# Kernel optimization log

Measured on AMD Instinct MI355X. Metric: run time of the kernel, lower is better.

The kernel has to match this reference:

```python
import jax, jax.numpy as jnp
import numpy as np

LN_EPS = 1e-5
OPM_EPS = 1e-3


def setup_inputs() -> dict:
    key = jax.random.key(0)
    ks = jax.random.split(key, 8)
    S, N, c_m, c_h, c_z = 128, 256, 256, 32, 128
    m = jax.random.normal(ks[0], (S, N, c_m), dtype=jnp.float32)
    mask = jnp.ones((S, N), dtype=jnp.float32)
    ln_w = jnp.ones((c_m,), dtype=jnp.float32)
    ln_b = jnp.zeros((c_m,), dtype=jnp.float32)
    sc1 = 1.0 / np.sqrt(c_m)
    w1 = jax.random.uniform(ks[1], (c_m, c_h), jnp.float32, -sc1, sc1)
    b1 = jax.random.uniform(ks[2], (c_h,), jnp.float32, -sc1, sc1)
    w2 = jax.random.uniform(ks[3], (c_m, c_h), jnp.float32, -sc1, sc1)
    b2 = jax.random.uniform(ks[4], (c_h,), jnp.float32, -sc1, sc1)
    sco = 1.0 / np.sqrt(c_h * c_h)
    wo = jax.random.uniform(ks[5], (c_h * c_h, c_z), jnp.float32, -sco, sco)
    bo = jax.random.uniform(ks[6], (c_z,), jnp.float32, -sco, sco)
    return {"m": m, "mask": mask, "ln_w": ln_w, "ln_b": ln_b,
            "w1": w1, "b1": b1, "w2": w2, "b2": b2, "wo": wo, "bo": bo}


def reference(m, mask, ln_w, ln_b, w1, b1, w2, b2, wo, bo):
    # LayerNorm over c_m
    mu = jnp.mean(m, axis=-1, keepdims=True)
    var = jnp.var(m, axis=-1, keepdims=True)
    ln = (m - mu) * jax.lax.rsqrt(var + LN_EPS) * ln_w + ln_b
    mk = mask[..., None]                       # [S, N, 1]
    a = (ln @ w1 + b1) * mk                    # [S, N, c_h]
    b = (ln @ w2 + b2) * mk                    # [S, N, c_h]
    # outer-product mean over the MSA dim s: [N, N, c_h, c_h]
    S, N, ch = a.shape
    outer = jnp.einsum('sic,sjd->ijcd', a, b).reshape(N, N, ch * ch)
    outer = outer @ wo + bo                    # [N, N, c_z]
    norm = jnp.einsum('si,sj->ij', mask, mask)[..., None] + OPM_EPS
    return outer / norm
```

## Files before the change

### kernel.cpp

```cpp
#include <hip/hip_runtime.h>
#include <hip/hip_bf16.h>

typedef __attribute__((ext_vector_type(8))) short short8;
typedef __attribute__((ext_vector_type(4))) short short4v;
typedef __attribute__((ext_vector_type(4))) float float4v;

#define S_DIM 128
#define N_DIM 256
#define CM    256
#define CH    32
#define CZ    128

#define AS1 __attribute__((address_space(1)))
#define AS3 __attribute__((address_space(3)))

static __device__ __forceinline__ short f2bf(float v) {
    return __builtin_bit_cast(short, __float2bfloat16(v));
}


__global__ __launch_bounds__(256) void prep_aux_kernel(
    const float* __restrict__ m, const float* __restrict__ mask,
    const float* __restrict__ lnw, const float* __restrict__ lnb,
    const float* __restrict__ w1, const float* __restrict__ b1,
    const float* __restrict__ w2, const float* __restrict__ b2,
    const float* __restrict__ wo, const float* __restrict__ bo,
    __hip_bfloat16* __restrict__ a_f, __hip_bfloat16* __restrict__ b_f,
    __hip_bfloat16* __restrict__ wo_f, float* __restrict__ ninv)
{
    __shared__ __align__(16) char lds_raw[77824];
    __hip_bfloat16* ln_lds = (__hip_bfloat16*)lds_raw;
    __hip_bfloat16* w_lds  = (__hip_bfloat16*)(lds_raw + 33792);
    __hip_bfloat16* st_lds = (__hip_bfloat16*)(lds_raw + 67584);

    const int bid = blockIdx.x, t = threadIdx.x;

    if (bid >= 576) {
        int i0 = (bid - 576) * 4, j = t;
        float a0 = 0.f, a1 = 0.f, a2 = 0.f, a3 = 0.f;
        for (int s = 0; s < S_DIM; ++s) {
            float mj = mask[s * N_DIM + j];
            a0 += mask[s * N_DIM + i0 + 0] * mj;
            a1 += mask[s * N_DIM + i0 + 1] * mj;
            a2 += mask[s * N_DIM + i0 + 2] * mj;
            a3 += mask[s * N_DIM + i0 + 3] * mj;
        }
        ninv[(i0 + 0) * N_DIM + j] = 1.0f / (a0 + 1e-3f);
        ninv[(i0 + 1) * N_DIM + j] = 1.0f / (a1 + 1e-3f);
        ninv[(i0 + 2) * N_DIM + j] = 1.0f / (a2 + 1e-3f);
        ninv[(i0 + 3) * N_DIM + j] = 1.0f / (a3 + 1e-3f);
        return;
    }
    if (bid >= 512) {
        int fidx = (bid - 512) * 256 + t;
        int l  = fidx & 63;
        int d  = (fidx >> 6) & 31;
        int zt = fidx >> 11;
        int z  = zt * 16 + (l & 15);
        int cb = (l >> 4) * 8;
        short8 frag;
        #pragma unroll
        for (int j = 0; j < 8; ++j)
            frag[j] = f2bf(wo[(size_t)((cb + j) * 32 + d) * CZ + z]);
        *(short8*)&wo_f[(size_t)fidx * 8] = frag;
        return;
    }

    const int lane = t & 63, wv = t >> 6;
    const int q = lane >> 4, c16 = lane & 15;
    const int n0 = (bid & 127) * 2, s0 = (bid >> 7) * 32, sk = bid >> 7;

    #pragma unroll 4
    for (int i = 0; i < 64; ++i) {
        int e = i * 256 + t;
        int k = e >> 6, c = e & 63;
        float v = (c < CH) ? w1[k * CH + c] : w2[k * CH + (c - CH)];
        w_lds[c * 264 + k] = __float2bfloat16(v);
    }

    float4 lw = ((const float4*)lnw)[lane];
    float4 lb = ((const float4*)lnb)[lane];

    #pragma unroll 2
    for (int it = 0; it < 16; ++it) {
        int rl = wv * 16 + it;
        int r  = (s0 + (rl >> 1)) * N_DIM + n0 + (rl & 1);
        float4 mv = ((const float4*)(m + (size_t)r * CM))[lane];
        float s1 = mv.x + mv.y + mv.z + mv.w;
        float s2 = mv.x*mv.x + mv.y*mv.y + mv.z*mv.z + mv.w*mv.w;
        #pragma unroll
        for (int o = 32; o > 0; o >>= 1) {
            s1 += __shfl_xor(s1, o, 64);
            s2 += __shfl_xor(s2, o, 64);
        }
        float mu  = s1 * (1.0f / 256.0f);
        float var = s2 * (1.0f / 256.0f) - mu * mu;
        float rs  = rsqrtf(var + 1e-5f);
        int base = rl * 264 + lane * 4;
        ln_lds[base + 0] = __float2bfloat16((mv.x - mu) * rs * lw.x + lb.x);
        ln_lds[base + 1] = __float2bfloat16((mv.y - mu) * rs * lw.y + lb.y);
        ln_lds[base + 2] = __float2bfloat16((mv.z - mu) * rs * lw.z + lb.z);
        ln_lds[base + 3] = __float2bfloat16((mv.w - mu) * rs * lw.w + lb.w);
    }
    __syncthreads();

    float4v acc[4];
    #pragma unroll
    for (int ct = 0; ct < 4; ++ct) acc[ct] = (float4v){0.f, 0.f, 0.f, 0.f};
    #pragma unroll
    for (int ks = 0; ks < 8; ++ks) {
        int k0 = ks * 32 + q * 8;
        short8 af = *(const short8*)&ln_lds[(wv * 16 + c16) * 264 + k0];
        #pragma unroll
        for (int ct = 0; ct < 4; ++ct) {
            short8 wb = *(const short8*)&w_lds[(ct * 16 + c16) * 264 + k0];
            acc[ct] = __builtin_amdgcn_mfma_f32_16x16x32_bf16(af, wb, acc[ct], 0, 0, 0);
        }
    }

    #pragma unroll
    for (int ct = 0; ct < 4; ++ct) {
        int cc = ct * 16 + c16;
        float bias = (cc < CH) ? b1[cc] : b2[cc - CH];
        #pragma unroll
        for (int rr = 0; rr < 4; ++rr) {
            int rl = wv * 16 + q * 4 + rr;
            int r  = (s0 + (rl >> 1)) * N_DIM + n0 + (rl & 1);
            float val = (acc[ct][rr] + bias) * mask[r];
            st_lds[((rl & 1) * 64 + cc) * 40 + (rl >> 1)] = __float2bfloat16(val);
        }
    }
    __syncthreads();

    #pragma unroll
    for (int i = 0; i < 2; ++i) {
        int slot = i * 256 + t;
        int f8 = slot >> 6, l = slot & 63;
        int fl = f8 & 3, nl = fl >> 1, cch = fl & 1;
        int lq = l >> 4, lc16 = l & 15;
        int col = nl * 64 + (f8 >= 4 ? 32 : 0) + cch * 16 + lc16;
        short8 v = *(const short8*)&st_lds[col * 40 + lq * 8];
        __hip_bfloat16* base = (f8 >= 4) ? b_f : a_f;
        *(short8*)&base[(size_t)((n0 * 2 + fl) * 4 + sk) * 512 + l * 8] = v;
    }
}

__global__ __launch_bounds__(512, 4) void main_kernel(
    const __hip_bfloat16* __restrict__ a_f, const __hip_bfloat16* __restrict__ b_f,
    const __hip_bfloat16* __restrict__ wo_f, const float* __restrict__ bo,
    const float* __restrict__ ninv, float* __restrict__ out)
{
    __shared__ __align__(16) short lds[33280];

    const int t = threadIdx.x, l = t & 63, wv = t >> 6;
    const int q = l >> 4, c16 = l & 15;
    const int bi = blockIdx.x, bj0 = blockIdx.y * 2;
    const size_t Ix = (size_t)bi * 8;

    #pragma unroll
    for (int tau = 0; tau < 2; ++tau) {
        const size_t Jx = (size_t)(bj0 + tau) * 8;
        #pragma unroll
        for (int i = 0; i < 4; ++i) {
            int f = i * 8 + wv;
            __builtin_amdgcn_global_load_lds(
                (AS1 const void*)&b_f[((Jx + (f >> 2)) * 4 + (f & 3)) * 512 + l * 8],
                (AS3 void*)&lds[tau * 16640 + f * 512], 16, 0, 0);
        }
    }

    const int tauW = wv & 1, Ig = (wv >> 1) & 1, Jg = wv >> 2;
    const int RB = tauW * 16640;

    float4v acc[4][4];
    #pragma unroll
    for (int ii = 0; ii < 4; ++ii)
        #pragma unroll
        for (int jj = 0; jj < 4; ++jj)
            acc[ii][jj] = (float4v){0.f, 0.f, 0.f, 0.f};

    __syncthreads();

    #pragma unroll 1
    for (int sk = 0; sk < 4; ++sk) {
        short8 afr[4], bfr[4];
        #pragma unroll
        for (int ii = 0; ii < 4; ++ii)
            afr[ii] = *(const short8*)&a_f[((Ix + Ig * 4 + ii) * 4 + sk) * 512 + l * 8];
        #pragma unroll
        for (int jj = 0; jj < 4; ++jj)
            bfr[jj] = *(const short8*)&lds[RB + ((Jg * 4 + jj) * 4 + sk) * 512 + l * 8];
        #pragma unroll
        for (int jj = 0; jj < 4; ++jj)
            #pragma unroll
            for (int ii = 0; ii < 4; ++ii)
                acc[ii][jj] = __builtin_amdgcn_mfma_f32_16x16x32_bf16(afr[ii], bfr[jj], acc[ii][jj], 0, 0, 0);
    }
    __syncthreads();

    #pragma unroll
    for (int ii = 0; ii < 4; ++ii) {
        const int c0 = (ii & 1) * 16 + q * 4;
        #pragma unroll
        for (int jj = 0; jj < 4; ++jj) {
            const int d = (jj & 1) * 16 + c16;
            const int p = (Ig * 2 + (ii >> 1)) * 4 + Jg * 2 + (jj >> 1);
            short4v pk;
            #pragma unroll
            for (int rr = 0; rr < 4; ++rr) pk[rr] = f2bf(acc[ii][jj][rr]);
            *(short4v*)&lds[RB + d * 520 + (c0 >> 3) * 128 + p * 8 + (c0 & 7)] = pk;
        }
    }
    __syncthreads();

    const int zt = wv & 3, kh = wv >> 2;
    float4v oa00 = (float4v){0.f, 0.f, 0.f, 0.f};
    float4v oa01 = oa00, oa10 = oa00, oa11 = oa00;
    #pragma unroll 2
    for (int d16 = 0; d16 < 16; ++d16) {
        const int d = kh * 16 + d16;
        short8 p0 = *(const short8*)&lds[d * 520 + l * 8];
        short8 p1 = *(const short8*)&lds[16640 + d * 520 + l * 8];
        short8 w0 = *(const short8*)&wo_f[(size_t)(zt * 64 + d) * 512 + l * 8];
        short8 w1 = *(const short8*)&wo_f[(size_t)(zt * 64 + 32 + d) * 512 + l * 8];
        oa00 = __builtin_amdgcn_mfma_f32_16x16x32_bf16(p0, w0, oa00, 0, 0, 0);
        oa01 = __builtin_amdgcn_mfma_f32_16x16x32_bf16(p0, w1, oa01, 0, 0, 0);
        oa10 = __builtin_amdgcn_mfma_f32_16x16x32_bf16(p1, w0, oa10, 0, 0, 0);
        oa11 = __builtin_amdgcn_mfma_f32_16x16x32_bf16(p1, w1, oa11, 0, 0, 0);
    }
    __syncthreads();

    float* red = (float*)lds;
    const int slot = (zt * 64 + l) * 4;
    if (kh) {
        *(float4v*)&red[slot]        = oa00;
        *(float4v*)&red[1024 + slot] = oa01;
    } else {
        *(float4v*)&red[2048 + slot] = oa10;
        *(float4v*)&red[3072 + slot] = oa11;
    }
    __syncthreads();

    float4v f0, f1;
    if (kh == 0) {
        f0 = oa00 + *(const float4v*)&red[slot];
        f1 = oa01 + *(const float4v*)&red[1024 + slot];
    } else {
        f0 = oa10 + *(const float4v*)&red[2048 + slot];
        f1 = oa11 + *(const float4v*)&red[3072 + slot];
    }

    const int gi = bi * 4 + q;
    const int bj = bj0 + kh;
    const int z0 = zt * 32 + c16;
    const float bz0 = bo[z0], bz1 = bo[z0 + 16];
    #pragma unroll
    for (int rr = 0; rr < 4; ++rr) {
        const int gj = bj * 4 + rr;
        const float nv = ninv[gi * N_DIM + gj];
        float* o = &out[((size_t)gi * N_DIM + gj) * CZ + z0];
        o[0]  = (f0[rr] + bz0) * nv;
        o[16] = (f1[rr] + bz1) * nv;
    }
}

extern "C" void kernel_launch(void* const* d_in, const int* in_sizes, int n_in,
                              void* d_out, int out_size, void* d_ws, size_t ws_size,
                              hipStream_t stream) {
    const float* m    = (const float*)d_in[0];
    const float* mask = (const float*)d_in[1];
    const float* lnw  = (const float*)d_in[2];
    const float* lnb  = (const float*)d_in[3];
    const float* w1   = (const float*)d_in[4];
    const float* b1   = (const float*)d_in[5];
    const float* w2   = (const float*)d_in[6];
    const float* b2   = (const float*)d_in[7];
    const float* wo   = (const float*)d_in[8];
    const float* bo   = (const float*)d_in[9];
    float* out = (float*)d_out;

    char* ws = (char*)d_ws;
    __hip_bfloat16* a_f  = (__hip_bfloat16*)ws;
    __hip_bfloat16* b_f  = (__hip_bfloat16*)(ws + (2u << 20));
    __hip_bfloat16* wo_f = (__hip_bfloat16*)(ws + (4u << 20));
    float*          ninv = (float*)(ws + (4u << 20) + (256u << 10));

    prep_aux_kernel<<<640, 256, 0, stream>>>(m, mask, lnw, lnb, w1, b1, w2, b2,
                                             wo, bo, a_f, b_f, wo_f, ninv);
    main_kernel<<<dim3(64, 32), 512, 0, stream>>>(a_f, b_f, wo_f, bo, ninv, out);
}
```

Before: 144.5 us.

## Enlarge main kernel tile to 8x8 residue pairs for operand reuse

```diff
diff --git a/kernel.cpp b/kernel.cpp
--- a/kernel.cpp
+++ b/kernel.cpp
@@ -145,122 +145,140 @@
     }
 }
 
-__global__ __launch_bounds__(512, 4) void main_kernel(
+__global__ __launch_bounds__(512, 2) void main_kernel(
     const __hip_bfloat16* __restrict__ a_f, const __hip_bfloat16* __restrict__ b_f,
     const __hip_bfloat16* __restrict__ wo_f, const float* __restrict__ bo,
     const float* __restrict__ ninv, float* __restrict__ out)
 {
-    __shared__ __align__(16) short lds[33280];
+    __shared__ __align__(16) short lds[66560];
 
     const int t = threadIdx.x, l = t & 63, wv = t >> 6;
     const int q = l >> 4, c16 = l & 15;
-    const int bi = blockIdx.x, bj0 = blockIdx.y * 2;
-    const size_t Ix = (size_t)bi * 8;
-
-    #pragma unroll
-    for (int tau = 0; tau < 2; ++tau) {
-        const size_t Jx = (size_t)(bj0 + tau) * 8;
-        #pragma unroll
-        for (int i = 0; i < 4; ++i) {
-            int f = i * 8 + wv;
-            __builtin_amdgcn_global_load_lds(
-                (AS1 const void*)&b_f[((Jx + (f >> 2)) * 4 + (f & 3)) * 512 + l * 8],
-                (AS3 void*)&lds[tau * 16640 + f * 512], 16, 0, 0);
-        }
-    }
-
-    const int tauW = wv & 1, Ig = (wv >> 1) & 1, Jg = wv >> 2;
-    const int RB = tauW * 16640;
-
-    float4v acc[4][4];
+    const int bi = blockIdx.x, bj = blockIdx.y;
+    const size_t Ix = (size_t)bi * 16;
+    const size_t Jx = (size_t)bj * 16;
+
+    #pragma unroll
+    for (int i = 0; i < 8; ++i) {
+        int f = i * 8 + wv;
+        __builtin_amdgcn_global_load_lds(
+            (AS1 const void*)&b_f[((Jx + (f >> 2)) * 4 + (f & 3)) * 512 + l * 8],
+            (AS3 void*)&lds[f * 512], 16, 0, 0);
+    }
+
+    const int wr = wv & 1, wc = wv >> 1;
+
+    short8 af[4][4];
     #pragma unroll
     for (int ii = 0; ii < 4; ++ii)
         #pragma unroll
-        for (int jj = 0; jj < 4; ++jj)
-            acc[ii][jj] = (float4v){0.f, 0.f, 0.f, 0.f};
-
-    __syncthreads();
-
-    #pragma unroll 1
-    for (int sk = 0; sk < 4; ++sk) {
-        short8 afr[4], bfr[4];
+        for (int sk = 0; sk < 4; ++sk)
+            af[ii][sk] = *(const short8*)&a_f[((Ix + wr * 4 + ii) * 4 + sk) * 512 + l * 8];
+
+    __syncthreads();
+
+    #pragma unroll
+    for (int h = 0; h < 2; ++h) {
+        float4v acc[4][4];
         #pragma unroll
         for (int ii = 0; ii < 4; ++ii)
-            afr[ii] = *(const short8*)&a_f[((Ix + Ig * 4 + ii) * 4 + sk) * 512 + l * 8];
-        #pragma unroll
-        for (int jj = 0; jj < 4; ++jj)
-            bfr[jj] = *(const short8*)&lds[RB + ((Jg * 4 + jj) * 4 + sk) * 512 + l * 8];
-        #pragma unroll
-        for (int jj = 0; jj < 4; ++jj)
+            #pragma unroll
+            for (int jj = 0; jj < 4; ++jj)
+                acc[ii][jj] = (float4v){0.f, 0.f, 0.f, 0.f};
+
+        #pragma unroll 1
+        for (int sk = 0; sk < 4; ++sk) {
+            short8 bfr[4];
+            #pragma unroll
+            for (int jj = 0; jj < 4; ++jj)
+                bfr[jj] = *(const short8*)&lds[((wc * 4 + jj) * 4 + sk) * 512 + l * 8];
+            #pragma unroll
+            for (int jj = 0; jj < 4; ++jj)
+                #pragma unroll
+                for (int ii = 0; ii < 4; ++ii)
+                    acc[ii][jj] = __builtin_amdgcn_mfma_f32_16x16x32_bf16(af[ii][sk], bfr[jj], acc[ii][jj], 0, 0, 0);
+        }
+
+        if (h == 0) {
             #pragma unroll
             for (int ii = 0; ii < 4; ++ii)
-                acc[ii][jj] = __builtin_amdgcn_mfma_f32_16x16x32_bf16(afr[ii], bfr[jj], acc[ii][jj], 0, 0, 0);
-    }
-    __syncthreads();
-
-    #pragma unroll
-    for (int ii = 0; ii < 4; ++ii) {
-        const int c0 = (ii & 1) * 16 + q * 4;
-        #pragma unroll
-        for (int jj = 0; jj < 4; ++jj) {
-            const int d = (jj & 1) * 16 + c16;
-            const int p = (Ig * 2 + (ii >> 1)) * 4 + Jg * 2 + (jj >> 1);
-            short4v pk;
-            #pragma unroll
-            for (int rr = 0; rr < 4; ++rr) pk[rr] = f2bf(acc[ii][jj][rr]);
-            *(short4v*)&lds[RB + d * 520 + (c0 >> 3) * 128 + p * 8 + (c0 & 7)] = pk;
+                #pragma unroll
+                for (int sk = 0; sk < 4; ++sk)
+                    af[ii][sk] = *(const short8*)&a_f[((Ix + 8 + wr * 4 + ii) * 4 + sk) * 512 + l * 8];
+        } else {
+            __syncthreads();
+        }
+
+        const int ib = h * 4;
+        #pragma unroll
+        for (int ii = 0; ii < 4; ++ii) {
+            const int i_loc = ib + ((wr * 4 + ii) >> 1);
+            const int c0 = (ii & 1) * 16 + q * 4;
+            #pragma unroll
+            for (int jj = 0; jj < 4; ++jj) {
+                const int j_loc = (wc * 4 + jj) >> 1;
+                const int d = (jj & 1) * 16 + c16;
+                const int pair = i_loc * 8 + j_loc;
+                const int pf = pair >> 4, p = pair & 15;
+                short4v pk;
+                #pragma unroll
+                for (int rr = 0; rr < 4; ++rr) pk[rr] = f2bf(acc[ii][jj][rr]);
+                *(short4v*)&lds[(((pf + 2) & 3) * 32 + d) * 520 + (c0 >> 3) * 128 + p * 8 + (c0 & 7)] = pk;
+            }
         }
     }
     __syncthreads();
 
     const int zt = wv & 3, kh = wv >> 2;
-    float4v oa00 = (float4v){0.f, 0.f, 0.f, 0.f};
-    float4v oa01 = oa00, oa10 = oa00, oa11 = oa00;
+    float4v oacc[4][2];
+    #pragma unroll
+    for (int pf = 0; pf < 4; ++pf) {
+        oacc[pf][0] = (float4v){0.f, 0.f, 0.f, 0.f};
+        oacc[pf][1] = (float4v){0.f, 0.f, 0.f, 0.f};
+    }
     #pragma unroll 2
     for (int d16 = 0; d16 < 16; ++d16) {
         const int d = kh * 16 + d16;
-        short8 p0 = *(const short8*)&lds[d * 520 + l * 8];
-        short8 p1 = *(const short8*)&lds[16640 + d * 520 + l * 8];
-        short8 w0 = *(const short8*)&wo_f[(size_t)(zt * 64 + d) * 512 + l * 8];
-        short8 w1 = *(const short8*)&wo_f[(size_t)(zt * 64 + 32 + d) * 512 + l * 8];
-        oa00 = __builtin_amdgcn_mfma_f32_16x16x32_bf16(p0, w0, oa00, 0, 0, 0);
-        oa01 = __builtin_amdgcn_mfma_f32_16x16x32_bf16(p0, w1, oa01, 0, 0, 0);
-        oa10 = __builtin_amdgcn_mfma_f32_16x16x32_bf16(p1, w0, oa10, 0, 0, 0);
-        oa11 = __builtin_amdgcn_mfma_f32_16x16x32_bf16(p1, w1, oa11, 0, 0, 0);
+        short8 w0 = *(const short8*)&wo_f[(size_t)((zt * 2 + 0) * 32 + d) * 512 + l * 8];
+        short8 w1 = *(const short8*)&wo_f[(size_t)((zt * 2 + 1) * 32 + d) * 512 + l * 8];
+        short8 pfr[4];
+        #pragma unroll
+        for (int pf = 0; pf < 4; ++pf)
+            pfr[pf] = *(const short8*)&lds[(((pf + 2) & 3) * 32 + d) * 520 + l * 8];
+        #pragma unroll
+        for (int pf = 0; pf < 4; ++pf) {
+            oacc[pf][0] = __builtin_amdgcn_mfma_f32_16x16x32_bf16(pfr[pf], w0, oacc[pf][0], 0, 0, 0);
+            oacc[pf][1] = __builtin_amdgcn_mfma_f32_16x16x32_bf16(pfr[pf], w1, oacc[pf][1], 0, 0, 0);
+        }
     }
     __syncthreads();
 
     float* red = (float*)lds;
-    const int slot = (zt * 64 + l) * 4;
-    if (kh) {
-        *(float4v*)&red[slot]        = oa00;
-        *(float4v*)&red[1024 + slot] = oa01;
-    } else {
-        *(float4v*)&red[2048 + slot] = oa10;
-        *(float4v*)&red[3072 + slot] = oa11;
-    }
-    __syncthreads();
-
-    float4v f0, f1;
-    if (kh == 0) {
-        f0 = oa00 + *(const float4v*)&red[slot];
-        f1 = oa01 + *(const float4v*)&red[1024 + slot];
-    } else {
-        f0 = oa10 + *(const float4v*)&red[2048 + slot];
-        f1 = oa11 + *(const float4v*)&red[3072 + slot];
-    }
-
-    const int gi = bi * 4 + q;
-    const int bj = bj0 + kh;
+    #pragma unroll
+    for (int pfo = 0; pfo < 2; ++pfo) {
+        const int pf = (1 - kh) * 2 + pfo;
+        *(float4v*)&red[(((zt * 2 + 0) * 4 + pf) * 64 + l) * 4] = oacc[pf][0];
+        *(float4v*)&red[(((zt * 2 + 1) * 4 + pf) * 64 + l) * 4] = oacc[pf][1];
+    }
+    __syncthreads();
+
     const int z0 = zt * 32 + c16;
     const float bz0 = bo[z0], bz1 = bo[z0 + 16];
     #pragma unroll
-    for (int rr = 0; rr < 4; ++rr) {
-        const int gj = bj * 4 + rr;
-        const float nv = ninv[gi * N_DIM + gj];
-        float* o = &out[((size_t)gi * N_DIM + gj) * CZ + z0];
-        o[0]  = (f0[rr] + bz0) * nv;
-        o[16] = (f1[rr] + bz1) * nv;
+    for (int pfo = 0; pfo < 2; ++pfo) {
+        const int pf = kh * 2 + pfo;
+        float4v s0 = oacc[pf][0] + *(const float4v*)&red[(((zt * 2 + 0) * 4 + pf) * 64 + l) * 4];
+        float4v s1 = oacc[pf][1] + *(const float4v*)&red[(((zt * 2 + 1) * 4 + pf) * 64 + l) * 4];
+        #pragma unroll
+        for (int rr = 0; rr < 4; ++rr) {
+            const int pair = pf * 16 + q * 4 + rr;
+            const int gi = bi * 8 + (pair >> 3);
+            const int gj = bj * 8 + (pair & 7);
+            const float nv = ninv[gi * N_DIM + gj];
+            float* o = &out[((size_t)gi * N_DIM + gj) * CZ + z0];
+            o[0]  = (s0[rr] + bz0) * nv;
+            o[16] = (s1[rr] + bz1) * nv;
+        }
     }
 }
 
@@ -287,5 +305,5 @@
 
     prep_aux_kernel<<<640, 256, 0, stream>>>(m, mask, lnw, lnb, w1, b1, w2, b2,
                                              wo, bo, a_f, b_f, wo_f, ninv);
-    main_kernel<<<dim3(64, 32), 512, 0, stream>>>(a_f, b_f, wo_f, bo, ninv, out);
+    main_kernel<<<dim3(32, 32), 512, 0, stream>>>(a_f, b_f, wo_f, bo, ninv, out);
 }
```

New measurement: 246.2 us. +70.4%, slower.
